# Kernel optimization log

Hardware: AMD Instinct MI355X
Metric: run time of the kernel (lower is better)

Reference implementation:

```python
import jax, jax.numpy as jnp
import numpy as np

H = 64  # hidden size hard-coded in the torch module


def _lstm_cell(x, h, c, Wih, Whh, b):
    # PyTorch LSTMCell: gates = x @ Wih.T + h @ Whh.T + bias_ih + bias_hh,
    # gate order (i, f, g, o), each of size H.
    gates = x @ Wih.T + h @ Whh.T + b
    i, f, g, o = jnp.split(gates, 4, axis=-1)
    c_new = jax.nn.sigmoid(f) * c + jax.nn.sigmoid(i) * jnp.tanh(g)
    h_new = jax.nn.sigmoid(o) * jnpp_tanh(c_new) if False else jax.nn.sigmoid(o) * jnp.tanh(c_new)
    return h_new, c_new


def setup_inputs() -> dict:
    key = jax.random.key(0)
    ks = jax.random.split(key, 12)
    B, T, F = 2048, 1024, 1
    s = 1.0 / np.sqrt(H)  # PyTorch LSTMCell/Linear init range

    def u(k, shape):
        return jax.random.uniform(k, shape, jnp.float32, -s, s)

    return {
        "input": jax.random.normal(ks[0], (B, T, F), jnp.float32),
        "Wih1": u(ks[1], (4 * H, F)),
        "Whh1": u(ks[2], (4 * H, H)),
        "bih1": u(ks[3], (4 * H,)),
        "bhh1": u(ks[4], (4 * H,)),
        "Wih2": u(ks[5], (4 * H, H)),
        "Whh2": u(ks[6], (4 * H, H)),
        "bih2": u(ks[7], (4 * H,)),
        "bhh2": u(ks[8], (4 * H,)),
        "Wl": u(ks[9], (1, H)),
        "bl": u(ks[10], (1,)),
        "future": 8,
    }


def reference(input, Wih1, Whh1, bih1, bhh1, Wih2, Whh2, bih2, bhh2, Wl, bl, future):
    B = input.shape[0]
    dtype = input.dtype
    z = jnp.zeros((B, H), dtype)
    b1 = bih1 + bhh1
    b2 = bih2 + bhh2

    def step(carry, x_t):
        h1, c1, h2, c2 = carry
        h1, c1 = _lstm_cell(x_t, h1, c1, Wih1, Whh1, b1)
        h2, c2 = _lstm_cell(h1, h2, c2, Wih2, Whh2, b2)
        return (h1, c1, h2, c2), None

    # scan over time: xs shaped [T, B, F]
    (h1, c1, h2, c2), _ = jax.lax.scan(step, (z, z, z, z), jnp.swapaxes(input, 0, 1))
    out = h2 @ Wl.T + bl  # readout from last input step

    def fstep(carry, _):
        out, h1, c1, h2, c2 = carry
        h1, c1 = _lstm_cell(out, h1, c1, Wih1, Whh1, b1)
        h2, c2 = _lstm_cell(h1, h2, c2, Wih2, Whh2, b2)
        out = h2 @ Wl.T + bl
        return (out, h1, c1, h2, c2), None

    (out, h1, c1, h2, c2), _ = jax.lax.scan(fstep, (out, h1, c1, h2, c2), None, length=future)
    return out[:, None, :]  # [B, 1, out_feature]
```

## Files before the change

### kernel.cpp

```cpp
#include <hip/hip_runtime.h>

#define HID 64
#define TSTEPS 1024
#define BPW 8
#define TW 512

typedef __attribute__((ext_vector_type(8))) short short8v;
typedef __attribute__((ext_vector_type(4))) float f32x4;

__device__ __forceinline__ unsigned short f2bf(float f) {
  unsigned u = __float_as_uint(f);
  u += 0x7FFFu + ((u >> 16) & 1u);
  return (unsigned short)(u >> 16);
}
__device__ __forceinline__ float bf2f(unsigned short h) {
  return __uint_as_float(((unsigned)h) << 16);
}
__device__ __forceinline__ float sigf(float x) {
  return __builtin_amdgcn_rcpf(1.0f + __expf(-x));
}
__device__ __forceinline__ float tanh_(float x) {
  return 1.0f - 2.0f * __builtin_amdgcn_rcpf(1.0f + __expf(2.0f * x));
}
__device__ __forceinline__ float dppror8(float x) {
  int xi = __float_as_int(x);
  int y = __builtin_amdgcn_update_dpp(xi, xi, 0x128, 0xF, 0xF, true);
  return __int_as_float(y);
}
__device__ __forceinline__ f32x4 mf(short8v a, short8v b, f32x4 c) {
  return __builtin_amdgcn_mfma_f32_16x16x32_bf16(a, b, c, 0, 0, 0);
}
__device__ __forceinline__ unsigned cvtpk_bf16(float a) {
  unsigned r;
  asm("v_cvt_pk_bf16_f32 %0, %1, %2" : "=v"(r) : "v"(a), "v"(a));
  return r;
}
__device__ __forceinline__ short8v ld_frag(const short* buf, int ss, int lane) {
  int byte = (ss * 64 + lane) * 16;
  byte ^= ((byte >> 7) & 7) << 4;
  return *(const short8v*)((const char*)buf + byte);
}
__device__ __forceinline__ int frag_addr16(int j, int col) {
  int byte = ((j >> 5) * 64 + ((j & 31) >> 3) * 16 + col) * 16 + (j & 7) * 2;
  byte ^= ((byte >> 7) & 7) << 4;
  return byte;
}
__device__ __forceinline__ void load8split(const float* rp, short8v& hi, short8v& lo) {
  float t[8];
#pragma unroll
  for (int e = 0; e < 8; ++e) t[e] = rp[e];
#pragma unroll
  for (int e = 0; e < 8; ++e) {
    unsigned short h = f2bf(t[e]);
    hi[e] = (short)h;
    lo[e] = (short)f2bf(t[e] - bf2f(h));
  }
}
__device__ __forceinline__ float cellup(float zi, float zf, float zg, float zo,
                                        float& c) {
  c = sigf(zf) * c + sigf(zi) * tanh_(zg);
  return sigf(zo) * tanh_(c);
}
__device__ __forceinline__ void fold2(const f32x4& a0, const f32x4& a1,
                                      bool dsel, float (&z)[4]) {
#pragma unroll
  for (int q = 0; q < 4; ++q) {
    float send = dsel ? a0[q] : a1[q];
    float own = dsel ? a1[q] : a0[q];
    z[q] = own + dppror8(send);
  }
}

struct __align__(128) SMem {
  float xin[TSTEPS + 1][BPW];
  short hf1[2][1024];
  short hf2[2][1024];
  float ro[8][BPW];
};

#define PINV(v) asm volatile("" : "+v"(v))

__global__ __launch_bounds__(TW, 2) void lstm2_kernel(
    const float* __restrict__ input, const float* __restrict__ Wih1,
    const float* __restrict__ Whh1, const float* __restrict__ bih1,
    const float* __restrict__ bhh1, const float* __restrict__ Wih2,
    const float* __restrict__ Whh2, const float* __restrict__ bih2,
    const float* __restrict__ bhh2, const float* __restrict__ Wl,
    const float* __restrict__ bl, const int* __restrict__ future,
    float* __restrict__ out) {
  __shared__ SMem s;
  const int tid = threadIdx.x;
  const int w = tid >> 6;
  const int lane = tid & 63;
  const int c = lane & 15;
  const int b = c & 7;
  const int d = (c >> 3) & 1;
  const int g = lane >> 4;
  const int jl = 4 * (2 * w + d) + g;
  const int b0 = blockIdx.x * BPW;

  short8v W1h[2][2], W1l[2][2];
  short8v W2h[2][2], W2l[2][2];
  short8v W3h[2][2], W3l[2][2];
#pragma unroll
  for (int tt = 0; tt < 2; ++tt) {
    const int T = 2 * w + tt;
    const int r16 = lane & 15;
    const int m = 64 * (r16 & 3) + 4 * T + (r16 >> 2);
    const int koff = (lane >> 4) * 8;
#pragma unroll
    for (int ss = 0; ss < 2; ++ss) {
      load8split(Whh1 + m * HID + ss * 32 + koff, W1h[tt][ss], W1l[tt][ss]);
      load8split(Wih2 + m * HID + ss * 32 + koff, W2h[tt][ss], W2l[tt][ss]);
      load8split(Whh2 + m * HID + ss * 32 + koff, W3h[tt][ss], W3l[tt][ss]);
    }
  }
#pragma unroll
  for (int tt = 0; tt < 2; ++tt)
#pragma unroll
    for (int ss = 0; ss < 2; ++ss) {
      PINV(W1h[tt][ss]); PINV(W1l[tt][ss]);
      PINV(W2h[tt][ss]); PINV(W2l[tt][ss]);
      PINV(W3h[tt][ss]); PINV(W3l[tt][ss]);
    }

  float bb1[4], wi1[4], bb2[4];
#pragma unroll
  for (int q = 0; q < 4; ++q) {
    const int row = 64 * q + jl;
    bb1[q] = bih1[row] + bhh1[row];
    wi1[q] = Wih1[row];
    bb2[q] = bih2[row] + bhh2[row];
  }
  const float wlv = Wl[jl];
  const float blv = bl[0];
  const int nfut = future[0];
  const int adr_hi = frag_addr16(jl, b);
  const int adr_lo = frag_addr16(jl, b + 8);

  {
    const float* src = input + (size_t)b0 * TSTEPS;
    for (int idx = tid; idx < BPW * TSTEPS; idx += TW) {
      int bi = idx >> 10;
      int t = idx & (TSTEPS - 1);
      s.xin[t][bi] = src[idx];
    }
    for (int idx = tid; idx < 2 * 1024; idx += TW) {
      ((short*)s.hf1)[idx] = 0;
      ((short*)s.hf2)[idx] = 0;
    }
  }
  const f32x4 zf = (f32x4){0.f, 0.f, 0.f, 0.f};
  f32x4 acc1_0 = zf, acc1_1 = zf;
  f32x4 acc2_0 = zf, acc2_1 = zf;
  float c1 = 0.f, c2 = 0.f;
  float h2n = 0.f;
  __syncthreads();

  const int total = TSTEPS + nfut;
  for (int sidx = 0; sidx < total; ++sidx) {
    const int p = sidx & 1, pn = p ^ 1;

    {
      short8v B0 = ld_frag(s.hf2[p], 0, lane);
      short8v B1 = ld_frag(s.hf2[p], 1, lane);
      acc2_0 = mf(W3h[0][1], B1,
                  mf(W3l[0][1], B1, mf(W3h[0][0], B0, mf(W3l[0][0], B0, zf))));
      acc2_1 = mf(W3h[1][1], B1,
                  mf(W3l[1][1], B1, mf(W3h[1][0], B0, mf(W3l[1][0], B0, zf))));
    }
    {
      const int xt = (sidx < TSTEPS) ? sidx : TSTEPS;
      const float xv = s.xin[xt][b];
      float z[4];
      fold2(acc1_0, acc1_1, d, z);
#pragma unroll
      for (int q = 0; q < 4; ++q) z[q] += bb1[q] + xv * wi1[q];
      float h1n = cellup(z[0], z[1], z[2], z[3], c1);
      unsigned rh = cvtpk_bf16(h1n);
      float res = h1n - __uint_as_float(rh << 16);
      unsigned rl = cvtpk_bf16(res);
      char* hf1w = (char*)s.hf1[pn];
      *(short*)(hf1w + adr_hi) = (short)rh;
      *(short*)(hf1w + adr_lo) = (short)rl;
    }
    __syncthreads();

    {
      short8v C0 = ld_frag(s.hf1[pn], 0, lane);
      short8v C1 = ld_frag(s.hf1[pn], 1, lane);
      acc2_0 = mf(W2h[0][1], C1,
                  mf(W2l[0][1], C1, mf(W2h[0][0], C0, mf(W2l[0][0], C0, acc2_0))));
      acc2_1 = mf(W2h[1][1], C1,
                  mf(W2l[1][1], C1, mf(W2h[1][0], C0, mf(W2l[1][0], C0, acc2_1))));
      acc1_0 = mf(W1h[0][1], C1,
                  mf(W1l[0][1], C1, mf(W1h[0][0], C0, mf(W1l[0][0], C0, zf))));
      acc1_1 = mf(W1h[1][1], C1,
                  mf(W1l[1][1], C1, mf(W1h[1][0], C0, mf(W1l[1][0], C0, zf))));
      float z[4];
      fold2(acc2_0, acc2_1, d, z);
#pragma unroll
      for (int q = 0; q < 4; ++q) z[q] += bb2[q];
      h2n = cellup(z[0], z[1], z[2], z[3], c2);
      unsigned rh = cvtpk_bf16(h2n);
      float res = h2n - __uint_as_float(rh << 16);
      unsigned rl = cvtpk_bf16(res);
      char* hf2w = (char*)s.hf2[pn];
      *(short*)(hf2w + adr_hi) = (short)rh;
      *(short*)(hf2w + adr_lo) = (short)rl;
    }

    if (sidx >= TSTEPS - 1) {
      float v = wlv * h2n;
      v += __shfl_xor(v, 8, 64);
      v += __shfl_xor(v, 16, 64);
      v += __shfl_xor(v, 32, 64);
      if (lane < 8) s.ro[w][lane] = v;
      __syncthreads();
      if (tid < 8) {
        float t = blv;
#pragma unroll
        for (int k = 0; k < 8; ++k) t += s.ro[k][tid];
        s.xin[TSTEPS][tid] = t;
      }
    }
    __syncthreads();
  }

  if (tid < 8) out[b0 + tid] = s.xin[TSTEPS][tid];
}

extern "C" void kernel_launch(void* const* d_in, const int* in_sizes, int n_in,
                              void* d_out, int out_size, void* d_ws,
                              size_t ws_size, hipStream_t stream) {
  const float* input = (const float*)d_in[0];
  const float* Wih1 = (const float*)d_in[1];
  const float* Whh1 = (const float*)d_in[2];
  const float* bih1 = (const float*)d_in[3];
  const float* bhh1 = (const float*)d_in[4];
  const float* Wih2 = (const float*)d_in[5];
  const float* Whh2 = (const float*)d_in[6];
  const float* bih2 = (const float*)d_in[7];
  const float* bhh2 = (const float*)d_in[8];
  const float* Wl = (const float*)d_in[9];
  const float* bl = (const float*)d_in[10];
  const int* fut = (const int*)d_in[11];
  float* out = (float*)d_out;

  const int B = in_sizes[0] / TSTEPS;
  const int blocks = B / BPW;

  hipLaunchKernelGGL(lstm2_kernel, dim3(blocks), dim3(TW), 0, stream, input,
                     Wih1, Whh1, bih1, bhh1, Wih2, Whh2, bih2, bhh2, Wl, bl,
                     fut, out);
}
```

Measured before the change: 869.1 us.

## Skew LSTM layers so both cells update in one barrier phase per step

Restructures the recurrence into a skewed pipeline: at iteration i, layer 2 processes step i-1 while layer 1 processes step i, so all MFMA products come from the previous buffer. This cuts the barriers per time step from two to one and lets the six MFMA chains issue together. The readout reduction is folded into the future phase with an extra barrier. In exchange, per-iteration register pressure rises, and there is one extra iteration plus prologue/epilogue predication.

```diff
diff --git a/kernel.cpp b/kernel.cpp
--- a/kernel.cpp
+++ b/kernel.cpp
@@ -72,7 +72,7 @@
 }
 
 struct __align__(128) SMem {
-  float xin[TSTEPS + 1][BPW];
+  float xin[TSTEPS][BPW];
   short hf1[2][1024];
   short hf2[2][1024];
   float ro[8][BPW];
@@ -151,31 +151,73 @@
     }
   }
   const f32x4 zf = (f32x4){0.f, 0.f, 0.f, 0.f};
-  f32x4 acc1_0 = zf, acc1_1 = zf;
-  f32x4 acc2_0 = zf, acc2_1 = zf;
   float c1 = 0.f, c2 = 0.f;
-  float h2n = 0.f;
   __syncthreads();
 
   const int total = TSTEPS + nfut;
-  for (int sidx = 0; sidx < total; ++sidx) {
-    const int p = sidx & 1, pn = p ^ 1;
-
-    {
-      short8v B0 = ld_frag(s.hf2[p], 0, lane);
-      short8v B1 = ld_frag(s.hf2[p], 1, lane);
-      acc2_0 = mf(W3h[0][1], B1,
-                  mf(W3l[0][1], B1, mf(W3h[0][0], B0, mf(W3l[0][0], B0, zf))));
-      acc2_1 = mf(W3h[1][1], B1,
-                  mf(W3l[1][1], B1, mf(W3h[1][0], B0, mf(W3l[1][0], B0, zf))));
-    }
-    {
-      const int xt = (sidx < TSTEPS) ? sidx : TSTEPS;
-      const float xv = s.xin[xt][b];
+  for (int i = 0; i <= total; ++i) {
+    const int p = i & 1, pn = p ^ 1;
+    const bool doL1 = (i < total);
+    const bool doL2 = (i >= 1);
+    const bool fut = (i >= TSTEPS);
+
+    short8v C0 = ld_frag(s.hf1[p], 0, lane);
+    short8v C1 = ld_frag(s.hf1[p], 1, lane);
+    short8v B0 = ld_frag(s.hf2[p], 0, lane);
+    short8v B1 = ld_frag(s.hf2[p], 1, lane);
+
+    f32x4 a1_0 = mf(W1h[0][1], C1,
+                    mf(W1l[0][1], C1, mf(W1h[0][0], C0, mf(W1l[0][0], C0, zf))));
+    f32x4 a1_1 = mf(W1h[1][1], C1,
+                    mf(W1l[1][1], C1, mf(W1h[1][0], C0, mf(W1l[1][0], C0, zf))));
+    f32x4 aA_0 = mf(W3h[0][1], B1,
+                    mf(W3l[0][1], B1, mf(W3h[0][0], B0, mf(W3l[0][0], B0, zf))));
+    f32x4 aA_1 = mf(W3h[1][1], B1,
+                    mf(W3l[1][1], B1, mf(W3h[1][0], B0, mf(W3l[1][0], B0, zf))));
+    f32x4 aB_0 = mf(W2h[0][1], C1,
+                    mf(W2l[0][1], C1, mf(W2h[0][0], C0, mf(W2l[0][0], C0, zf))));
+    f32x4 aB_1 = mf(W2h[1][1], C1,
+                    mf(W2l[1][1], C1, mf(W2h[1][0], C0, mf(W2l[1][0], C0, zf))));
+
+    if (doL2) {
+      f32x4 s0 = aA_0 + aB_0;
+      f32x4 s1 = aA_1 + aB_1;
       float z[4];
-      fold2(acc1_0, acc1_1, d, z);
-#pragma unroll
-      for (int q = 0; q < 4; ++q) z[q] += bb1[q] + xv * wi1[q];
+      fold2(s0, s1, d, z);
+#pragma unroll
+      for (int q = 0; q < 4; ++q) z[q] += bb2[q];
+      float h2n = cellup(z[0], z[1], z[2], z[3], c2);
+      unsigned rh = cvtpk_bf16(h2n);
+      float res = h2n - __uint_as_float(rh << 16);
+      unsigned rl = cvtpk_bf16(res);
+      char* hf2w = (char*)s.hf2[pn];
+      *(short*)(hf2w + adr_hi) = (short)rh;
+      *(short*)(hf2w + adr_lo) = (short)rl;
+      if (fut) {
+        float v = wlv * h2n;
+        v += __shfl_xor(v, 8, 64);
+        v += __shfl_xor(v, 16, 64);
+        v += __shfl_xor(v, 32, 64);
+        if (lane < 8) s.ro[w][lane] = v;
+      }
+    }
+
+    float x = 0.0f;
+    if (fut) {
+      __syncthreads();
+      float t = blv;
+#pragma unroll
+      for (int k = 0; k < 8; ++k) t += s.ro[k][b];
+      x = t;
+    } else {
+      x = s.xin[i][b];
+    }
+
+    if (doL1) {
+      float z[4];
+      fold2(a1_0, a1_1, d, z);
+#pragma unroll
+      for (int q = 0; q < 4; ++q) z[q] += bb1[q] + x * wi1[q];
       float h1n = cellup(z[0], z[1], z[2], z[3], c1);
       unsigned rh = cvtpk_bf16(h1n);
       float res = h1n - __uint_as_float(rh << 16);
@@ -185,49 +227,14 @@
       *(short*)(hf1w + adr_lo) = (short)rl;
     }
     __syncthreads();
-
-    {
-      short8v C0 = ld_frag(s.hf1[pn], 0, lane);
-      short8v C1 = ld_frag(s.hf1[pn], 1, lane);
-      acc2_0 = mf(W2h[0][1], C1,
-                  mf(W2l[0][1], C1, mf(W2h[0][0], C0, mf(W2l[0][0], C0, acc2_0))));
-      acc2_1 = mf(W2h[1][1], C1,
-                  mf(W2l[1][1], C1, mf(W2h[1][0], C0, mf(W2l[1][0], C0, acc2_1))));
-      acc1_0 = mf(W1h[0][1], C1,
-                  mf(W1l[0][1], C1, mf(W1h[0][0], C0, mf(W1l[0][0], C0, zf))));
-      acc1_1 = mf(W1h[1][1], C1,
-                  mf(W1l[1][1], C1, mf(W1h[1][0], C0, mf(W1l[1][0], C0, zf))));
-      float z[4];
-      fold2(acc2_0, acc2_1, d, z);
-#pragma unroll
-      for (int q = 0; q < 4; ++q) z[q] += bb2[q];
-      h2n = cellup(z[0], z[1], z[2], z[3], c2);
-      unsigned rh = cvtpk_bf16(h2n);
-      float res = h2n - __uint_as_float(rh << 16);
-      unsigned rl = cvtpk_bf16(res);
-      char* hf2w = (char*)s.hf2[pn];
-      *(short*)(hf2w + adr_hi) = (short)rh;
-      *(short*)(hf2w + adr_lo) = (short)rl;
-    }
-
-    if (sidx >= TSTEPS - 1) {
-      float v = wlv * h2n;
-      v += __shfl_xor(v, 8, 64);
-      v += __shfl_xor(v, 16, 64);
-      v += __shfl_xor(v, 32, 64);
-      if (lane < 8) s.ro[w][lane] = v;
-      __syncthreads();
-      if (tid < 8) {
-        float t = blv;
-#pragma unroll
-        for (int k = 0; k < 8; ++k) t += s.ro[k][tid];
-        s.xin[TSTEPS][tid] = t;
-      }
-    }
-    __syncthreads();
-  }
-
-  if (tid < 8) out[b0 + tid] = s.xin[TSTEPS][tid];
+  }
+
+  if (tid < 8) {
+    float t = blv;
+#pragma unroll
+    for (int k = 0; k < 8; ++k) t += s.ro[k][tid];
+    out[b0 + tid] = t;
+  }
 }
 
 extern "C" void kernel_launch(void* const* d_in, const int* in_sizes, int n_in,
```

Result: slower. 948.1 us (+9.1%).

## Skew layer pipeline across 16 waves so both LSTM cells update together

Applied to the files above, without the earlier changes.

Doubles the block to 1024 threads and gives each wave one gate tile instead of two. Lanes with d=0 now compute the layer-1 cell while lanes with d=1 compute the layer-2 cell for the previous step, so one barrier per step replaces the serial layer-1 then layer-2 phases. The change aims to halve the per-step MFMA and transcendental work on each wave and to shorten the dependency chain. In exchange it adds an extra pipeline iteration, a selection between the two layers in each lane, and a barrier inside the readout during the future steps. It also raises block-level synchronisation cost and puts tighter demands on registers and occupancy.

```diff
diff --git a/kernel.cpp b/kernel.cpp
--- a/kernel.cpp
+++ b/kernel.cpp
@@ -3,7 +3,7 @@
 #define HID 64
 #define TSTEPS 1024
 #define BPW 8
-#define TW 512
+#define TW 1024
 
 typedef __attribute__((ext_vector_type(8))) short short8v;
 typedef __attribute__((ext_vector_type(4))) float f32x4;
@@ -56,11 +56,6 @@
     lo[e] = (short)f2bf(t[e] - bf2f(h));
   }
 }
-__device__ __forceinline__ float cellup(float zi, float zf, float zg, float zo,
-                                        float& c) {
-  c = sigf(zf) * c + sigf(zi) * tanh_(zg);
-  return sigf(zo) * tanh_(c);
-}
 __device__ __forceinline__ void fold2(const f32x4& a0, const f32x4& a1,
                                       bool dsel, float (&z)[4]) {
 #pragma unroll
@@ -72,15 +67,15 @@
 }
 
 struct __align__(128) SMem {
-  float xin[TSTEPS + 1][BPW];
+  float xin[TSTEPS][BPW];
   short hf1[2][1024];
   short hf2[2][1024];
-  float ro[8][BPW];
+  float ro[16][BPW];
 };
 
 #define PINV(v) asm volatile("" : "+v"(v))
 
-__global__ __launch_bounds__(TW, 2) void lstm2_kernel(
+__global__ __launch_bounds__(TW, 4) void lstm2_kernel(
     const float* __restrict__ input, const float* __restrict__ Wih1,
     const float* __restrict__ Whh1, const float* __restrict__ bih1,
     const float* __restrict__ bhh1, const float* __restrict__ Wih2,
@@ -96,43 +91,38 @@
   const int b = c & 7;
   const int d = (c >> 3) & 1;
   const int g = lane >> 4;
-  const int jl = 4 * (2 * w + d) + g;
+  const int jl = 4 * w + g;
   const int b0 = blockIdx.x * BPW;
 
-  short8v W1h[2][2], W1l[2][2];
-  short8v W2h[2][2], W2l[2][2];
-  short8v W3h[2][2], W3l[2][2];
-#pragma unroll
-  for (int tt = 0; tt < 2; ++tt) {
-    const int T = 2 * w + tt;
+  short8v W1h[2], W1l[2];
+  short8v W2h[2], W2l[2];
+  short8v W3h[2], W3l[2];
+  {
     const int r16 = lane & 15;
-    const int m = 64 * (r16 & 3) + 4 * T + (r16 >> 2);
-    const int koff = (lane >> 4) * 8;
+    const int m = 64 * (r16 & 3) + 4 * w + (r16 >> 2);
+    const int koff = g * 8;
 #pragma unroll
     for (int ss = 0; ss < 2; ++ss) {
-      load8split(Whh1 + m * HID + ss * 32 + koff, W1h[tt][ss], W1l[tt][ss]);
-      load8split(Wih2 + m * HID + ss * 32 + koff, W2h[tt][ss], W2l[tt][ss]);
-      load8split(Whh2 + m * HID + ss * 32 + koff, W3h[tt][ss], W3l[tt][ss]);
-    }
-  }
-#pragma unroll
-  for (int tt = 0; tt < 2; ++tt)
-#pragma unroll
-    for (int ss = 0; ss < 2; ++ss) {
-      PINV(W1h[tt][ss]); PINV(W1l[tt][ss]);
-      PINV(W2h[tt][ss]); PINV(W2l[tt][ss]);
-      PINV(W3h[tt][ss]); PINV(W3l[tt][ss]);
-    }
-
-  float bb1[4], wi1[4], bb2[4];
+      load8split(Whh1 + m * HID + ss * 32 + koff, W1h[ss], W1l[ss]);
+      load8split(Wih2 + m * HID + ss * 32 + koff, W2h[ss], W2l[ss]);
+      load8split(Whh2 + m * HID + ss * 32 + koff, W3h[ss], W3l[ss]);
+    }
+  }
+#pragma unroll
+  for (int ss = 0; ss < 2; ++ss) {
+    PINV(W1h[ss]); PINV(W1l[ss]);
+    PINV(W2h[ss]); PINV(W2l[ss]);
+    PINV(W3h[ss]); PINV(W3l[ss]);
+  }
+
+  float bsel[4], wsel[4];
 #pragma unroll
   for (int q = 0; q < 4; ++q) {
     const int row = 64 * q + jl;
-    bb1[q] = bih1[row] + bhh1[row];
-    wi1[q] = Wih1[row];
-    bb2[q] = bih2[row] + bhh2[row];
-  }
-  const float wlv = Wl[jl];
+    bsel[q] = d ? (bih2[row] + bhh2[row]) : (bih1[row] + bhh1[row]);
+    wsel[q] = d ? 0.0f : Wih1[row];
+  }
+  const float wlv = d ? Wl[jl] : 0.0f;
   const float blv = bl[0];
   const int nfut = future[0];
   const int adr_hi = frag_addr16(jl, b);
@@ -151,83 +141,73 @@
     }
   }
   const f32x4 zf = (f32x4){0.f, 0.f, 0.f, 0.f};
-  f32x4 acc1_0 = zf, acc1_1 = zf;
-  f32x4 acc2_0 = zf, acc2_1 = zf;
-  float c1 = 0.f, c2 = 0.f;
-  float h2n = 0.f;
+  f32x4 accP = zf;
+  f32x4 accQ1 = zf;
+  f32x4 accQ2 = zf;
+  float cc = 0.f;
   __syncthreads();
 
   const int total = TSTEPS + nfut;
-  for (int sidx = 0; sidx < total; ++sidx) {
-    const int p = sidx & 1, pn = p ^ 1;
-
+  for (int i = 0; i <= total; ++i) {
+    const int pn = i & 1;
+
+    f32x4 aq = accQ1 + accQ2;
+    float z[4];
+    fold2(accP, aq, d, z);
+#pragma unroll
+    for (int q = 0; q < 4; ++q) z[q] += bsel[q];
+    float hnew, cnew;
+    if (i < TSTEPS) {
+      const float x = s.xin[i][b];
+#pragma unroll
+      for (int q = 0; q < 4; ++q) z[q] = fmaf(x, wsel[q], z[q]);
+      cnew = sigf(z[1]) * cc + sigf(z[0]) * tanh_(z[2]);
+      hnew = sigf(z[3]) * tanh_(cnew);
+    } else {
+      float cp = sigf(z[1]) * cc + sigf(z[0]) * tanh_(z[2]);
+      float hp = sigf(z[3]) * tanh_(cp);
+      float v = wlv * hp;
+      v += __shfl_xor(v, 16, 64);
+      v += __shfl_xor(v, 32, 64);
+      if (lane >= 8 && lane < 16) s.ro[w][lane - 8] = v;
+      __syncthreads();
+      float x = blv;
+#pragma unroll
+      for (int k = 0; k < 16; ++k) x += s.ro[k][b];
+#pragma unroll
+      for (int q = 0; q < 4; ++q) z[q] = fmaf(x, wsel[q], z[q]);
+      cnew = sigf(z[1]) * cc + sigf(z[0]) * tanh_(z[2]);
+      hnew = sigf(z[3]) * tanh_(cnew);
+    }
+    if (i == 0 && d) { cnew = 0.f; hnew = 0.f; }
+    cc = cnew;
     {
-      short8v B0 = ld_frag(s.hf2[p], 0, lane);
-      short8v B1 = ld_frag(s.hf2[p], 1, lane);
-      acc2_0 = mf(W3h[0][1], B1,
-                  mf(W3l[0][1], B1, mf(W3h[0][0], B0, mf(W3l[0][0], B0, zf))));
-      acc2_1 = mf(W3h[1][1], B1,
-                  mf(W3l[1][1], B1, mf(W3h[1][0], B0, mf(W3l[1][0], B0, zf))));
-    }
-    {
-      const int xt = (sidx < TSTEPS) ? sidx : TSTEPS;
-      const float xv = s.xin[xt][b];
-      float z[4];
-      fold2(acc1_0, acc1_1, d, z);
-#pragma unroll
-      for (int q = 0; q < 4; ++q) z[q] += bb1[q] + xv * wi1[q];
-      float h1n = cellup(z[0], z[1], z[2], z[3], c1);
-      unsigned rh = cvtpk_bf16(h1n);
-      float res = h1n - __uint_as_float(rh << 16);
+      unsigned rh = cvtpk_bf16(hnew);
+      float res = hnew - __uint_as_float(rh << 16);
       unsigned rl = cvtpk_bf16(res);
-      char* hf1w = (char*)s.hf1[pn];
-      *(short*)(hf1w + adr_hi) = (short)rh;
-      *(short*)(hf1w + adr_lo) = (short)rl;
+      short* hbuf = d ? s.hf2[pn] : s.hf1[pn];
+      *(short*)((char*)hbuf + adr_hi) = (short)rh;
+      *(short*)((char*)hbuf + adr_lo) = (short)rl;
     }
     __syncthreads();
 
-    {
+    if (i < total) {
       short8v C0 = ld_frag(s.hf1[pn], 0, lane);
       short8v C1 = ld_frag(s.hf1[pn], 1, lane);
-      acc2_0 = mf(W2h[0][1], C1,
-                  mf(W2l[0][1], C1, mf(W2h[0][0], C0, mf(W2l[0][0], C0, acc2_0))));
-      acc2_1 = mf(W2h[1][1], C1,
-                  mf(W2l[1][1], C1, mf(W2h[1][0], C0, mf(W2l[1][0], C0, acc2_1))));
-      acc1_0 = mf(W1h[0][1], C1,
-                  mf(W1l[0][1], C1, mf(W1h[0][0], C0, mf(W1l[0][0], C0, zf))));
-      acc1_1 = mf(W1h[1][1], C1,
-                  mf(W1l[1][1], C1, mf(W1h[1][0], C0, mf(W1l[1][0], C0, zf))));
-      float z[4];
-      fold2(acc2_0, acc2_1, d, z);
-#pragma unroll
-      for (int q = 0; q < 4; ++q) z[q] += bb2[q];
-      h2n = cellup(z[0], z[1], z[2], z[3], c2);
-      unsigned rh = cvtpk_bf16(h2n);
-      float res = h2n - __uint_as_float(rh << 16);
-      unsigned rl = cvtpk_bf16(res);
-      char* hf2w = (char*)s.hf2[pn];
-      *(short*)(hf2w + adr_hi) = (short)rh;
-      *(short*)(hf2w + adr_lo) = (short)rl;
-    }
-
-    if (sidx >= TSTEPS - 1) {
-      float v = wlv * h2n;
-      v += __shfl_xor(v, 8, 64);
-      v += __shfl_xor(v, 16, 64);
-      v += __shfl_xor(v, 32, 64);
-      if (lane < 8) s.ro[w][lane] = v;
-      __syncthreads();
-      if (tid < 8) {
-        float t = blv;
-#pragma unroll
-        for (int k = 0; k < 8; ++k) t += s.ro[k][tid];
-        s.xin[TSTEPS][tid] = t;
-      }
-    }
-    __syncthreads();
-  }
-
-  if (tid < 8) out[b0 + tid] = s.xin[TSTEPS][tid];
+      short8v D0 = ld_frag(s.hf2[pn], 0, lane);
+      short8v D1 = ld_frag(s.hf2[pn], 1, lane);
+      accP  = mf(W1h[1], C1, mf(W1l[1], C1, mf(W1h[0], C0, mf(W1l[0], C0, zf))));
+      accQ1 = mf(W2h[1], C1, mf(W2l[1], C1, mf(W2h[0], C0, mf(W2l[0], C0, zf))));
+      accQ2 = mf(W3h[1], D1, mf(W3l[1], D1, mf(W3h[0], D0, mf(W3l[0], D0, zf))));
+    }
+  }
+
+  if (tid < 8) {
+    float t = blv;
+#pragma unroll
+    for (int k = 0; k < 16; ++k) t += s.ro[k][tid];
+    out[b0 + tid] = t;
+  }
 }
 
 extern "C" void kernel_launch(void* const* d_in, const int* in_sizes, int n_in,
```

Result: slower. 911.4 us (+4.9%).
